# Kernel optimization log

Measured on AMD Instinct MI355X. Metric: run time of the kernel, lower is better.

The kernel has to match this reference:

```python
import jax
import jax.numpy as jnp
import numpy as np
from jax import lax

DIM = 48
HIDDEN = int(DIM * 2.66)  # 127, matches torch int(dim*ffn_expansion_factor)
EPS_LN = 1e-5
EPS_NORM = 1e-12


def conv2d(x, w, groups=1):
    # x: NCHW, w: OIHW, stride 1, SAME padding (all kernels here are 1x1 or 3x3 pad=1)
    return lax.conv_general_dilated(
        x, w, window_strides=(1, 1), padding='SAME',
        feature_group_count=groups,
        dimension_numbers=('NCHW', 'OIHW', 'NCHW'))


def layernorm_cbias(x, w, b):
    # Restormer WithBias_LayerNorm: normalize over channel dim (biased var)
    mu = jnp.mean(x, axis=1, keepdims=True)
    var = jnp.mean(jnp.square(x - mu), axis=1, keepdims=True)
    xn = (x - mu) * lax.rsqrt(var + EPS_LN)
    return xn * w[None, :, None, None] + b[None, :, None, None]


def l2norm_last(x):
    # torch F.normalize(dim=-1, eps=1e-12)
    n = jnp.sqrt(jnp.sum(jnp.square(x), axis=-1, keepdims=True))
    return x / jnp.maximum(n, EPS_NORM)


def setup_inputs() -> dict:
    key = jax.random.key(0)
    ks = jax.random.split(key, 16)
    s = 0.05
    B, H, W = 2, 512, 512
    return {
        'x': jax.random.normal(ks[0], (B, 3, H, W), dtype=jnp.float32),
        # OverlapPatchEmbed: Conv2d(3, 48, 3, pad=1, bias=False)
        'pe_w': jax.random.normal(ks[1], (DIM, 3, 3, 3), dtype=jnp.float32) * s,
        # norm1 (WithBias)
        'n1_w': jnp.ones((DIM,), dtype=jnp.float32),
        'n1_b': jnp.zeros((DIM,), dtype=jnp.float32),
        # MDTA attention, num_heads=1
        'temp': jnp.ones((1, 1, 1), dtype=jnp.float32),
        'qkv_w': jax.random.normal(ks[2], (DIM * 3, DIM, 1, 1), dtype=jnp.float32) * s,
        'qkv_dw_w': jax.random.normal(ks[3], (DIM * 3, 1, 3, 3), dtype=jnp.float32) * s,
        'po_w': jax.random.normal(ks[4], (DIM, DIM, 1, 1), dtype=jnp.float32) * s,
        # norm2
        'n2_w': jnp.ones((DIM,), dtype=jnp.float32),
        'n2_b': jnp.zeros((DIM,), dtype=jnp.float32),
        # GDFN
        'pi_w': jax.random.normal(ks[5], (HIDDEN * 2, DIM, 1, 1), dtype=jnp.float32) * s,
        'ffn_dw_w': jax.random.normal(ks[6], (HIDDEN * 2, 1, 3, 3), dtype=jnp.float32) * s,
        'fo_w': jax.random.normal(ks[7], (DIM, HIDDEN, 1, 1), dtype=jnp.float32) * s,
    }


def reference(x, pe_w, n1_w, n1_b, temp, qkv_w, qkv_dw_w, po_w, n2_w, n2_b, pi_w, ffn_dw_w, fo_w):
    # Patch embed
    patch = conv2d(x, pe_w)  # [B, 48, H, W]
    B, C, H, W = patch.shape

    # ---- MDTA channel attention on norm1(patch) ----
    y = layernorm_cbias(patch, n1_w, n1_b)
    qkv = conv2d(conv2d(y, qkv_w), qkv_dw_w, groups=3 * C)  # [B, 3C, H, W]
    q, k, v = jnp.split(qkv, 3, axis=1)
    # heads=1: rearrange to [B, C, H*W]
    q = l2norm_last(q.reshape(B, C, H * W))
    k = l2norm_last(k.reshape(B, C, H * W))
    v = v.reshape(B, C, H * W)
    attn = jax.nn.softmax(jnp.einsum('bcn,bdn->bcd', q, k) * temp[0, 0, 0], axis=-1)  # [B, C, C]
    out = jnp.einsum('bcd,bdn->bcn', attn, v).reshape(B, C, H, W)
    attn_out = conv2d(out, po_w)
    first = patch + attn_out

    # ---- GDFN on norm2(first) ----
    y2 = layernorm_cbias(first, n2_w, n2_b)
    h = conv2d(conv2d(y2, pi_w), ffn_dw_w, groups=2 * HIDDEN)  # [B, 254, H, W]
    x1, x2 = jnp.split(h, 2, axis=1)
    ffn = conv2d(jax.nn.gelu(x1, approximate=False) * x2, fo_w)
    return first + ffn  # second_residual [B, 48, H, W]
```

## Files before the change

kernel.cpp:

```cpp
#include <hip/hip_runtime.h>
#include <hip/hip_bf16.h>
#include <math.h>

#define HW 512
#define NPIX (HW*HW)

typedef __hip_bfloat16 bf16;
typedef __attribute__((ext_vector_type(8))) unsigned short u16x8;
typedef __attribute__((ext_vector_type(8))) short s16x8;
typedef __attribute__((ext_vector_type(4))) float f32x4;

__device__ __forceinline__ float b2f(bf16 v) { return __bfloat162float(v); }
__device__ __forceinline__ bf16 f2b(float v) { return __float2bfloat16(v); }

union fu { float f; unsigned int u; };
union bu { bf16 b; unsigned short u; };

__device__ __forceinline__ float us2f(unsigned short u) {
    fu c; c.u = ((unsigned int)u) << 16; return c.f;
}

__device__ __forceinline__ void ld_bf8(const bf16* p, float* f) {
    u16x8 u = *(const u16x8*)p;
#pragma unroll
    for (int j = 0; j < 8; j++) { fu c; c.u = ((unsigned int)u[j]) << 16; f[j] = c.f; }
}

__device__ __forceinline__ void st_bf8(bf16* p, const float* f) {
    u16x8 u;
#pragma unroll
    for (int j = 0; j < 8; j++) { bu c; c.b = f2b(f[j]); u[j] = c.u; }
    *(u16x8*)p = u;
}

__global__ __launch_bounds__(256) void k_prep(const float* __restrict__ qkvw,
                                              const float* __restrict__ piw,
                                              const float* __restrict__ fow,
                                              bf16* __restrict__ WQ,
                                              bf16* __restrict__ WP,
                                              bf16* __restrict__ WF,
                                              float* __restrict__ Z0,
                                              float* __restrict__ Z1)
{
    int idx = blockIdx.x*256 + threadIdx.x;
    if (idx < 9216) {
        int oc = idx >> 6, k = idx & 63;
        WQ[idx] = f2b(k < 48 ? qkvw[oc*48 + k] : 0.f);
    } else if (idx < 25600) {
        int j = idx - 9216; int oc = j >> 6, k = j & 63;
        WP[j] = f2b((oc < 254 && k < 48) ? piw[oc*48 + k] : 0.f);
    } else if (idx < 31744) {
        int j = idx - 25600; int oc = j >> 7, k = j & 127;
        WF[j] = f2b(k < 127 ? fow[oc*127 + k] : 0.f);
    } else if (idx < 36544) {
        int j = idx - 31744;
        if (j < 2400) Z0[j] = 0.f; else Z1[j-2400] = 0.f;
    }
}

__global__ __launch_bounds__(256) void k_pe(const float* __restrict__ x,
                                            const float* __restrict__ w,
                                            bf16* __restrict__ out)
{
    __shared__ float ws[48*27];
    for (int i = threadIdx.x; i < 48*27; i += 256) ws[i] = w[i];
    __syncthreads();
    int lane = threadIdx.x & 63, wv = threadIdx.x >> 6;
    int row = blockIdx.x*4 + wv;
    int col = lane*8;
    float a[3][3][8];
    float lf[3][3], rt[3][3];
#pragma unroll
    for (int c = 0; c < 3; c++)
#pragma unroll
        for (int r = 0; r < 3; r++) {
            int rr = row + r - 1;
            if (rr >= 0 && rr < HW) {
                const float* p = x + (size_t)c*NPIX + rr*HW + col;
                float4 u0 = *(const float4*)p, u1 = *(const float4*)(p+4);
                a[c][r][0]=u0.x; a[c][r][1]=u0.y; a[c][r][2]=u0.z; a[c][r][3]=u0.w;
                a[c][r][4]=u1.x; a[c][r][5]=u1.y; a[c][r][6]=u1.z; a[c][r][7]=u1.w;
            } else {
#pragma unroll
                for (int j = 0; j < 8; j++) a[c][r][j] = 0.f;
            }
            float l = __shfl_up(a[c][r][7], 1);  lf[c][r] = (lane==0)  ? 0.f : l;
            float rv= __shfl_down(a[c][r][0],1); rt[c][r] = (lane==63) ? 0.f : rv;
        }
    for (int oc = 0; oc < 48; oc++) {
        float acc[8];
#pragma unroll
        for (int j = 0; j < 8; j++) acc[j] = 0.f;
#pragma unroll
        for (int c = 0; c < 3; c++)
#pragma unroll
            for (int r = 0; r < 3; r++) {
                float w0 = ws[oc*27 + c*9 + r*3 + 0];
                float w1 = ws[oc*27 + c*9 + r*3 + 1];
                float w2 = ws[oc*27 + c*9 + r*3 + 2];
#pragma unroll
                for (int j = 0; j < 8; j++) {
                    float xm = (j==0) ? lf[c][r] : a[c][r][j-1];
                    float x0 = a[c][r][j];
                    float xp = (j==7) ? rt[c][r] : a[c][r][j+1];
                    acc[j] += w0*xm + w1*x0 + w2*xp;
                }
            }
        st_bf8(out + (size_t)oc*NPIX + row*HW + col, acc);
    }
}

#define YPAD 48
#define CHS 408
__global__ __launch_bounds__(256) void k_ln_dw(const bf16* __restrict__ patch,
                                               const float* __restrict__ lnw,
                                               const float* __restrict__ lnb,
                                               const s16x8* __restrict__ wq,
                                               const float* __restrict__ dww,
                                               bf16* __restrict__ outq)
{
    __shared__ unsigned short y_lds[400*YPAD];
    __shared__ unsigned short a_lds[48*CHS];
    int t = threadIdx.x;
    int c0 = blockIdx.x*32, r0 = blockIdx.y*8;

    for (int p = t; p < 400; p += 256) {
        int hr = p/40, hc = p - hr*40;
        int gr = r0 - 1 + hr, gc = c0 - 1 + hc;
        bool ok = (hc < 34) && (gr >= 0) && (gr < HW) && (gc >= 0) && (gc < HW);
        if (ok) {
            int gpx = gr*HW + gc;
            float y[48];
            float mu = 0.f;
#pragma unroll
            for (int i = 0; i < 48; i++) { y[i] = b2f(patch[(size_t)i*NPIX + gpx]); mu += y[i]; }
            mu *= (1.f/48.f);
            float var = 0.f;
#pragma unroll
            for (int i = 0; i < 48; i++) { float d = y[i]-mu; var += d*d; }
            float s = rsqrtf(var*(1.f/48.f) + 1e-5f);
#pragma unroll
            for (int i = 0; i < 48; i++) y[i] = (y[i]-mu)*s*lnw[i] + lnb[i];
#pragma unroll
            for (int kb = 0; kb < 6; kb++) {
                union { u16x8 v; unsigned short us[8]; } pk;
#pragma unroll
                for (int j = 0; j < 8; j++) { bu b; b.b = f2b(y[kb*8+j]); pk.us[j] = b.u; }
                *(u16x8*)&y_lds[p*YPAD + kb*8] = pk.v;
            }
        } else {
            u16x8 z = {0,0,0,0,0,0,0,0};
#pragma unroll
            for (int kb = 0; kb < 6; kb++) *(u16x8*)&y_lds[p*YPAD + kb*8] = z;
        }
    }
    __syncthreads();

    int lane = t & 63, wv = t >> 6;
    int q = lane >> 4, n = lane & 15;
    int ch2 = lane >> 5;
    int idx5 = lane & 31;
    int orow = idx5 >> 2;
    int cg   = idx5 & 3;

#pragma unroll 1
    for (int cc = 0; cc < 3; cc++) {
        s16x8 w0[3], w1[3];
#pragma unroll
        for (int mi = 0; mi < 3; mi++) {
            int oc = (cc*3 + mi)*16 + n;
            w0[mi] = wq[oc*8 + q];
            w1[mi] = wq[oc*8 + 4 + q];
        }
#pragma unroll 1
        for (int nt = wv; nt < 25; nt += 4) {
            int p16 = nt*16;
            s16x8 ya = *(const s16x8*)&y_lds[(p16 + n)*YPAD + q*8];
            s16x8 yb = {0,0,0,0,0,0,0,0};
            if (q < 2) yb = *(const s16x8*)&y_lds[(p16 + n)*YPAD + 32 + q*8];
#pragma unroll
            for (int mi = 0; mi < 3; mi++) {
                f32x4 acc = {0.f, 0.f, 0.f, 0.f};
                acc = __builtin_amdgcn_mfma_f32_16x16x32_bf16(ya, w0[mi], acc, 0, 0, 0);
                acc = __builtin_amdgcn_mfma_f32_16x16x32_bf16(yb, w1[mi], acc, 0, 0, 0);
                union { unsigned short us[4]; ushort4 v; } pk;
#pragma unroll
                for (int r = 0; r < 4; r++) { bu bb; bb.b = f2b(acc[r]); pk.us[r] = bb.u; }
                *(ushort4*)&a_lds[(mi*16 + n)*CHS + p16 + q*4] = pk.v;
            }
        }
        __syncthreads();

#pragma unroll 1
        for (int i = 0; i < 6; i++) {
            int chl = i*8 + wv*2 + ch2;
            int ch  = cc*48 + chl;
            float wk[9];
#pragma unroll
            for (int k = 0; k < 9; k++) wk[k] = dww[ch*9 + k];
            const unsigned short* ap = &a_lds[chl*CHS];
            float win[3][10];
#pragma unroll
            for (int kr = 0; kr < 3; kr++) {
                u16x8 A = *(const u16x8*)&ap[(orow + kr)*40 + cg*8];
                unsigned int B = *(const unsigned int*)&ap[(orow + kr)*40 + cg*8 + 8];
#pragma unroll
                for (int j = 0; j < 8; j++) win[kr][j] = us2f(A[j]);
                win[kr][8] = us2f((unsigned short)(B & 0xffffu));
                win[kr][9] = us2f((unsigned short)(B >> 16));
            }
            u16x8 pk;
#pragma unroll
            for (int j = 0; j < 8; j++) {
                float sm = 0.f;
#pragma unroll
                for (int kr = 0; kr < 3; kr++)
                    sm += wk[kr*3+0]*win[kr][j] + wk[kr*3+1]*win[kr][j+1] + wk[kr*3+2]*win[kr][j+2];
                bu b; b.b = f2b(sm); pk[j] = b.u;
            }
            *(u16x8*)&outq[(size_t)ch*NPIX + (r0 + orow)*HW + c0 + cg*8] = pk;
        }
        __syncthreads();
    }
}

template<int OC_PAD, int OC_REAL, int MT_PER_WAVE>
__global__ __launch_bounds__(256) void k_ln_mm_mfma(const bf16* __restrict__ in,
                                                    const float* __restrict__ lnw,
                                                    const float* __restrict__ lnb,
                                                    const s16x8* __restrict__ wpad,
                                                    bf16* __restrict__ out)
{
    constexpr int NMT = OC_PAD/16;
    __shared__ s16x8 y_lds[256*8];
    __shared__ unsigned short stage[OC_PAD][72];
    int t = threadIdx.x;
    int base = blockIdx.x*256;
    int px = base + t;
    float y[48];
    float mu = 0.f;
#pragma unroll
    for (int i = 0; i < 48; i++) { y[i] = b2f(in[(size_t)i*NPIX + px]); mu += y[i]; }
    mu *= (1.f/48.f);
    float var = 0.f;
#pragma unroll
    for (int i = 0; i < 48; i++) { float d = y[i]-mu; var += d*d; }
    float s = rsqrtf(var*(1.f/48.f) + 1e-5f);
#pragma unroll
    for (int i = 0; i < 48; i++) y[i] = (y[i]-mu)*s*lnw[i] + lnb[i];
#pragma unroll
    for (int kb = 0; kb < 8; kb++) {
        union { s16x8 v; unsigned short us[8]; } pk;
#pragma unroll
        for (int j = 0; j < 8; j++) {
            int c = kb*8 + j;
            bu b; b.b = f2b(c < 48 ? y[c] : 0.f);
            pk.us[j] = (c < 48) ? b.u : (unsigned short)0;
        }
        y_lds[t*8 + (kb ^ (t & 7))] = pk.v;
    }
    __syncthreads();

    int lane = t & 63, wv = t >> 6;
    int q = lane >> 4, n = lane & 15;
    s16x8 a[MT_PER_WAVE][2];
#pragma unroll
    for (int mi = 0; mi < MT_PER_WAVE; mi++) {
        int mt = wv + 4*mi;
        if (mt < NMT) {
            int oc = mt*16 + n;
            a[mi][0] = wpad[oc*8 + q];
            a[mi][1] = wpad[oc*8 + 4 + q];
        }
    }
#pragma unroll 1
    for (int g = 0; g < 4; g++) {
#pragma unroll
        for (int sub = 0; sub < 4; sub++) {
            int nt = g*4 + sub;
            int npx = nt*16 + n;
            s16x8 b0 = y_lds[npx*8 + (q ^ (npx & 7))];
            s16x8 b1 = y_lds[npx*8 + ((4 + q) ^ (npx & 7))];
#pragma unroll
            for (int mi = 0; mi < MT_PER_WAVE; mi++) {
                int mt = wv + 4*mi;
                if (mt >= NMT) continue;
                f32x4 acc = {0.f, 0.f, 0.f, 0.f};
                acc = __builtin_amdgcn_mfma_f32_16x16x32_bf16(b0, a[mi][0], acc, 0, 0, 0);
                acc = __builtin_amdgcn_mfma_f32_16x16x32_bf16(b1, a[mi][1], acc, 0, 0, 0);
                int oc = mt*16 + n;
                union { unsigned short us[4]; ushort4 v; } pk;
#pragma unroll
                for (int r = 0; r < 4; r++) { bu bb; bb.b = f2b(acc[r]); pk.us[r] = bb.u; }
                *(ushort4*)&stage[oc][sub*16 + q*4] = pk.v;
            }
        }
        __syncthreads();
        if (t < OC_REAL) {
            const u16x8* sp = (const u16x8*)stage[t];
            u16x8 c0 = sp[0], c1 = sp[1], c2 = sp[2], c3 = sp[3];
            u16x8 c4 = sp[4], c5 = sp[5], c6 = sp[6], c7 = sp[7];
            u16x8* op = (u16x8*)(out + (size_t)t*NPIX + base + g*64);
            op[0] = c0; op[1] = c1; op[2] = c2; op[3] = c3;
            op[4] = c4; op[5] = c5; op[6] = c6; op[7] = c7;
        }
        __syncthreads();
    }
}

__global__ __launch_bounds__(512) void k_qkt(const bf16* __restrict__ qm,
                                             const bf16* __restrict__ km,
                                             float* __restrict__ S,
                                             float* __restrict__ sumsq)
{
    __shared__ float Sp[8][48][52];
    __shared__ float ssp[8][96];
    int t = threadIdx.x;
    int lane = t & 63, wv = t >> 6;
    int qg = lane >> 4, n = lane & 15;
    size_t px0 = (size_t)(blockIdx.x*8 + wv) * 128 + qg*8;

    f32x4 acc[3][3];
#pragma unroll
    for (int i = 0; i < 3; i++)
#pragma unroll
        for (int j = 0; j < 3; j++) acc[i][j] = (f32x4){0.f, 0.f, 0.f, 0.f};
    float sq[3] = {0.f, 0.f, 0.f}, sk[3] = {0.f, 0.f, 0.f};

#pragma unroll 2
    for (int s = 0; s < 4; s++) {
        size_t p = px0 + s*32;
        s16x8 qa[3], ka[3];
#pragma unroll
        for (int i = 0; i < 3; i++) {
            qa[i] = *(const s16x8*)&qm[(size_t)(16*i + n)*NPIX + p];
            ka[i] = *(const s16x8*)&km[(size_t)(16*i + n)*NPIX + p];
        }
#pragma unroll
        for (int i = 0; i < 3; i++)
#pragma unroll
            for (int j = 0; j < 3; j++)
                acc[i][j] = __builtin_amdgcn_mfma_f32_16x16x32_bf16(qa[i], ka[j], acc[i][j], 0, 0, 0);
#pragma unroll
        for (int i = 0; i < 3; i++) {
            union { s16x8 v; unsigned short us[8]; } uq, uk;
            uq.v = qa[i]; uk.v = ka[i];
#pragma unroll
            for (int j = 0; j < 8; j++) {
                fu cq; cq.u = ((unsigned int)uq.us[j]) << 16; sq[i] += cq.f*cq.f;
                fu ck; ck.u = ((unsigned int)uk.us[j]) << 16; sk[i] += ck.f*ck.f;
            }
        }
    }

#pragma unroll
    for (int i = 0; i < 3; i++)
#pragma unroll
        for (int j = 0; j < 3; j++)
#pragma unroll
            for (int r = 0; r < 4; r++)
                Sp[wv][16*i + qg*4 + r][16*j + n] = acc[i][j][r];
#pragma unroll
    for (int i = 0; i < 3; i++) {
        float a = sq[i], b = sk[i];
        a += __shfl_down(a, 32); a += __shfl_down(a, 16);
        b += __shfl_down(b, 32); b += __shfl_down(b, 16);
        if (lane < 16) { ssp[wv][16*i + lane] = a; ssp[wv][48 + 16*i + lane] = b; }
    }
    __syncthreads();

    for (int idx = t; idx < 2304; idx += 512) {
        int r = idx / 48, c = idx - r*48;
        float v = 0.f;
#pragma unroll
        for (int w = 0; w < 8; w++) v += Sp[w][r][c];
        atomicAdd(&S[idx], v);
    }
    if (t < 96) {
        float v = 0.f;
#pragma unroll
        for (int w = 0; w < 8; w++) v += ssp[w][t];
        atomicAdd(&sumsq[t], v);
    }
}

__global__ __launch_bounds__(256) void k_attn_final(const float* __restrict__ S,
                                                    const float* __restrict__ sumsq,
                                                    const float* __restrict__ po_w,
                                                    const float* __restrict__ temp,
                                                    float* __restrict__ M)
{
    __shared__ float attn[48][48];
    __shared__ float nrm[96];
    int t = threadIdx.x;
    if (t < 96) nrm[t] = fmaxf(sqrtf(sumsq[t]), 1e-12f);
    __syncthreads();
    float tmp = temp[0];
    if (t < 48) {
        float row[48];
        float mx = -1e30f;
#pragma unroll
        for (int d = 0; d < 48; d++) {
            float l = S[t*48+d] / (nrm[t]*nrm[48+d]) * tmp;
            row[d] = l; mx = fmaxf(mx, l);
        }
        float sum = 0.f;
#pragma unroll
        for (int d = 0; d < 48; d++) { float e = expf(row[d]-mx); sum += e; row[d] = e; }
        float inv = 1.f/sum;
#pragma unroll
        for (int d = 0; d < 48; d++) attn[t][d] = row[d]*inv;
    }
    __syncthreads();
    for (int idx = t; idx < 2304; idx += 256) {
        int cp = idx/48, d = idx%48;
        float acc = 0.f;
#pragma unroll
        for (int c = 0; c < 48; c++) acc += po_w[cp*48+c] * attn[c][d];
        M[idx] = acc;
    }
}

__global__ __launch_bounds__(256) void k_attnv(const bf16* __restrict__ v,
                                               const float* __restrict__ M,
                                               bf16* __restrict__ patch)
{
    __shared__ float Ms[48*48];
    for (int i = threadIdx.x; i < 2304; i += 256) Ms[i] = M[i];
    __syncthreads();
    int p = (blockIdx.x*256 + threadIdx.x)*2;
    float v0[48], v1[48];
#pragma unroll
    for (int i = 0; i < 48; i++) {
        unsigned int word = *(const unsigned int*)&v[(size_t)i*NPIX + p];
        fu c0, c1; c0.u = word << 16; c1.u = word & 0xffff0000u;
        v0[i] = c0.f; v1[i] = c1.f;
    }
    for (int oc = 0; oc < 48; oc++) {
        const float4* wr = (const float4*)&Ms[oc*48];
        float a0 = 0.f, a1 = 0.f;
#pragma unroll
        for (int i = 0; i < 12; i++) {
            float4 w4 = wr[i];
            a0 += w4.x*v0[4*i] + w4.y*v0[4*i+1] + w4.z*v0[4*i+2] + w4.w*v0[4*i+3];
            a1 += w4.x*v1[4*i] + w4.y*v1[4*i+1] + w4.z*v1[4*i+2] + w4.w*v1[4*i+3];
        }
        unsigned int* pp = (unsigned int*)&patch[(size_t)oc*NPIX + p];
        unsigned int old = *pp;
        fu f0, f1; f0.u = old << 16; f1.u = old & 0xffff0000u;
        bu b0, b1; b0.b = f2b(f0.f + a0); b1.b = f2b(f1.f + a1);
        *pp = (unsigned int)b0.u | ((unsigned int)b1.u << 16);
    }
}

__global__ __launch_bounds__(256) void k_dw_glu(const bf16* __restrict__ h1,
                                                const float* __restrict__ w,
                                                bf16* __restrict__ g)
{
    int ch = blockIdx.y;
    int lane = threadIdx.x & 63, wv = threadIdx.x >> 6;
    int row0 = blockIdx.x*32 + wv*8;
    int col = lane*8;
    float w1[9], w2[9];
#pragma unroll
    for (int i = 0; i < 9; i++) { w1[i] = w[ch*9+i]; w2[i] = w[(ch+127)*9+i]; }
    const bf16* i1 = h1 + (size_t)ch*NPIX;
    const bf16* i2 = h1 + (size_t)(ch+127)*NPIX;
    bf16* op = g + (size_t)ch*NPIX;
    float aa[3][8], bb[3][8];
    float lfa[3], rta[3], lfb[3], rtb[3];

    auto loadrow = [&](int s, int rr) {
        if (rr >= 0 && rr < HW) {
            ld_bf8(i1 + rr*HW + col, aa[s]);
            ld_bf8(i2 + rr*HW + col, bb[s]);
        } else {
#pragma unroll
            for (int j = 0; j < 8; j++) { aa[s][j] = 0.f; bb[s][j] = 0.f; }
        }
        float l1 = __shfl_up(aa[s][7],1);   lfa[s] = (lane==0)  ? 0.f : l1;
        float r1 = __shfl_down(aa[s][0],1); rta[s] = (lane==63) ? 0.f : r1;
        float l2 = __shfl_up(bb[s][7],1);   lfb[s] = (lane==0)  ? 0.f : l2;
        float r2 = __shfl_down(bb[s][0],1); rtb[s] = (lane==63) ? 0.f : r2;
    };
    loadrow(0, row0-1);
    loadrow(1, row0);
#pragma unroll
    for (int r = 0; r < 8; r++) {
        loadrow((r+2)%3, row0 + r + 1);
        const int s0 = r%3, s1 = (r+1)%3, s2 = (r+2)%3;
        float o[8];
#pragma unroll
        for (int j = 0; j < 8; j++) {
            float sum1 = 0.f, sum2 = 0.f;
#pragma unroll
            for (int kr = 0; kr < 3; kr++) {
                const int ss = (kr==0) ? s0 : (kr==1) ? s1 : s2;
                float xm = (j==0) ? lfa[ss] : aa[ss][j-1];
                float x0 = aa[ss][j];
                float xp = (j==7) ? rta[ss] : aa[ss][j+1];
                sum1 += w1[kr*3+0]*xm + w1[kr*3+1]*x0 + w1[kr*3+2]*xp;
                float ym = (j==0) ? lfb[ss] : bb[ss][j-1];
                float y0 = bb[ss][j];
                float yp = (j==7) ? rtb[ss] : bb[ss][j+1];
                sum2 += w2[kr*3+0]*ym + w2[kr*3+1]*y0 + w2[kr*3+2]*yp;
            }
            float ge = 0.5f*sum1*(1.f + erff(sum1*0.70710678118654752f));
            o[j] = ge*sum2;
        }
        st_bf8(op + (row0 + r)*HW + col, o);
    }
}

__global__ __launch_bounds__(256) void k_fo_mfma(const bf16* __restrict__ g,
                                                 const s16x8* __restrict__ wfo,
                                                 const bf16* __restrict__ first,
                                                 float* __restrict__ out)
{
    __shared__ s16x8 glds[256*16];
    int t = threadIdx.x;
    int base = blockIdx.x*256;
    int px = base + t;
#pragma unroll
    for (int kb = 0; kb < 16; kb++) {
        union { s16x8 v; unsigned short us[8]; } pk;
#pragma unroll
        for (int j = 0; j < 8; j++) {
            int c = kb*8 + j;
            if (c < 127) { bu b; b.b = g[(size_t)c*NPIX + px]; pk.us[j] = b.u; }
            else pk.us[j] = 0;
        }
        glds[t*16 + (kb ^ (t & 15))] = pk.v;
    }
    __syncthreads();
    int lane = t & 63, wv = t >> 6;
    int q = lane >> 4, n = lane & 15;
    s16x8 a[3][4];
#pragma unroll
    for (int mt = 0; mt < 3; mt++) {
        int oc = mt*16 + n;
#pragma unroll
        for (int kc = 0; kc < 4; kc++)
            a[mt][kc] = wfo[oc*16 + kc*4 + q];
    }
#pragma unroll 1
    for (int ni = 0; ni < 4; ni++) {
        int nt = wv*4 + ni;
        int npx = nt*16 + n;
        s16x8 b[4];
#pragma unroll
        for (int kc = 0; kc < 4; kc++)
            b[kc] = glds[npx*16 + ((kc*4 + q) ^ (npx & 15))];
        size_t px4 = (size_t)base + nt*16 + q*4;
#pragma unroll
        for (int mt = 0; mt < 3; mt++) {
            f32x4 acc = {0.f, 0.f, 0.f, 0.f};
#pragma unroll
            for (int kc = 0; kc < 4; kc++)
                acc = __builtin_amdgcn_mfma_f32_16x16x32_bf16(b[kc], a[mt][kc], acc, 0, 0, 0);
            int oc = mt*16 + n;
            ushort4 fr = *(const ushort4*)&first[(size_t)oc*NPIX + px4];
            float4 o;
            o.x = us2f(fr.x) + acc[0];
            o.y = us2f(fr.y) + acc[1];
            o.z = us2f(fr.z) + acc[2];
            o.w = us2f(fr.w) + acc[3];
            *(float4*)&out[(size_t)oc*NPIX + px4] = o;
        }
    }
}

extern "C" void kernel_launch(void* const* d_in, const int* in_sizes, int n_in,
                              void* d_out, int out_size, void* d_ws, size_t ws_size,
                              hipStream_t stream)
{
    const float* x     = (const float*)d_in[0];
    const float* pe_w  = (const float*)d_in[1];
    const float* n1w   = (const float*)d_in[2];
    const float* n1b   = (const float*)d_in[3];
    const float* temp  = (const float*)d_in[4];
    const float* qkvw  = (const float*)d_in[5];
    const float* qkvdw = (const float*)d_in[6];
    const float* pow_  = (const float*)d_in[7];
    const float* n2w   = (const float*)d_in[8];
    const float* n2b   = (const float*)d_in[9];
    const float* piw   = (const float*)d_in[10];
    const float* ffndw = (const float*)d_in[11];
    const float* fow   = (const float*)d_in[12];
    float* out = (float*)d_out;

    bf16*  Pb = (bf16*)d_ws;
    bf16*  A  = Pb + (size_t)48*NPIX;
    bf16*  Bq = A + (size_t)144*NPIX;
    bf16*  H1 = A;
    bf16*  G  = A + (size_t)254*NPIX;
    bf16*  WQ = A + (size_t)381*NPIX;
    bf16*  WP = WQ + 144*64;
    bf16*  WF = WP + 256*64;
    float* SM0 = (float*)(A + (size_t)384*NPIX);
    float* SM1 = SM0 + 4704;

    dim3 blk(256);
    int nb1 = NPIX/256;
    int nb2 = NPIX/512;
    int nr  = HW/4;
    int nrw = HW/32;

    k_prep<<<dim3(143), blk, 0, stream>>>(qkvw, piw, fow, WQ, WP, WF, SM0, SM1);

    for (int b = 0; b < 2; b++) {
        const float* xb   = x   + (size_t)b*3*NPIX;
        float*       outb = out + (size_t)b*48*NPIX;
        float* SMb   = b ? SM1 : SM0;
        float* sumsq = SMb;
        float* S     = SMb + 96;
        float* M     = SMb + 2400;

        k_pe<<<dim3(nr), blk, 0, stream>>>(xb, pe_w, Pb);
        k_ln_dw<<<dim3(HW/32, HW/8), blk, 0, stream>>>(Pb, n1w, n1b, (const s16x8*)WQ, qkvdw, Bq);
        k_qkt<<<dim3(NPIX/1024), dim3(512), 0, stream>>>(Bq, Bq + (size_t)48*NPIX, S, sumsq);
        k_attn_final<<<dim3(1), blk, 0, stream>>>(S, sumsq, pow_, temp, M);
        k_attnv<<<dim3(nb2), blk, 0, stream>>>(Bq + (size_t)96*NPIX, M, Pb);
        k_ln_mm_mfma<256,254,4><<<dim3(nb1), blk, 0, stream>>>(Pb, n2w, n2b, (const s16x8*)WP, H1);
        k_dw_glu<<<dim3(nrw, 127), blk, 0, stream>>>(H1, ffndw, G);
        k_fo_mfma<<<dim3(nb1), blk, 0, stream>>>(G, (const s16x8*)WF, Pb, outb);
    }
}
```

Measured before the change: 749.3 us.

## Fuse depthwise GLU conv with output projection MFMA via LDS tile

Merges the depthwise 3x3 conv + GELU gating kernel with the fo 1x1 MFMA projection. Each block computes the gated hidden values for a 32x8 pixel tile across all 127 channels into shared memory, then runs the MFMA projection and residual add directly. This removes the round trip of the 127-channel intermediate G through global memory and one launch. In exchange it adds halo loads at tile edges, a large LDS footprint (~67KB) that limits occupancy, and strided LDS gathers for the B operand that may cause bank conflicts.

```diff
diff --git a/kernel.cpp b/kernel.cpp
--- a/kernel.cpp
+++ b/kernel.cpp
@@ -453,87 +453,90 @@
     }
 }
 
-__global__ __launch_bounds__(256) void k_dw_glu(const bf16* __restrict__ h1,
+#define GCHS 264
+__global__ __launch_bounds__(256) void k_glu_fo(const bf16* __restrict__ h1,
                                                 const float* __restrict__ w,
-                                                bf16* __restrict__ g)
-{
-    int ch = blockIdx.y;
-    int lane = threadIdx.x & 63, wv = threadIdx.x >> 6;
-    int row0 = blockIdx.x*32 + wv*8;
-    int col = lane*8;
-    float w1[9], w2[9];
-#pragma unroll
-    for (int i = 0; i < 9; i++) { w1[i] = w[ch*9+i]; w2[i] = w[(ch+127)*9+i]; }
-    const bf16* i1 = h1 + (size_t)ch*NPIX;
-    const bf16* i2 = h1 + (size_t)(ch+127)*NPIX;
-    bf16* op = g + (size_t)ch*NPIX;
-    float aa[3][8], bb[3][8];
-    float lfa[3], rta[3], lfb[3], rtb[3];
-
-    auto loadrow = [&](int s, int rr) {
-        if (rr >= 0 && rr < HW) {
-            ld_bf8(i1 + rr*HW + col, aa[s]);
-            ld_bf8(i2 + rr*HW + col, bb[s]);
-        } else {
-#pragma unroll
-            for (int j = 0; j < 8; j++) { aa[s][j] = 0.f; bb[s][j] = 0.f; }
-        }
-        float l1 = __shfl_up(aa[s][7],1);   lfa[s] = (lane==0)  ? 0.f : l1;
-        float r1 = __shfl_down(aa[s][0],1); rta[s] = (lane==63) ? 0.f : r1;
-        float l2 = __shfl_up(bb[s][7],1);   lfb[s] = (lane==0)  ? 0.f : l2;
-        float r2 = __shfl_down(bb[s][0],1); rtb[s] = (lane==63) ? 0.f : r2;
-    };
-    loadrow(0, row0-1);
-    loadrow(1, row0);
-#pragma unroll
-    for (int r = 0; r < 8; r++) {
-        loadrow((r+2)%3, row0 + r + 1);
-        const int s0 = r%3, s1 = (r+1)%3, s2 = (r+2)%3;
-        float o[8];
+                                                const s16x8* __restrict__ wfo,
+                                                const bf16* __restrict__ first,
+                                                float* __restrict__ out)
+{
+    __shared__ unsigned short g_lds[128*GCHS];
+    int t = threadIdx.x;
+    int lane = t & 63, wv = t >> 6;
+    int c0 = blockIdx.x*32, r0 = blockIdx.y*8;
+
+    int ch2 = lane >> 5;
+    int idx5 = lane & 31;
+    int orow = idx5 >> 2;
+    int cg   = idx5 & 3;
+    int col  = c0 + cg*8;
+
+#pragma unroll 1
+    for (int i = 0; i < 16; i++) {
+        int ch = i*8 + wv*2 + ch2;
+        bool valid = (ch < 127);
+        float w1[9], w2[9];
+#pragma unroll
+        for (int k = 0; k < 9; k++) {
+            w1[k] = valid ? w[ch*9+k] : 0.f;
+            w2[k] = valid ? w[(ch+127)*9+k] : 0.f;
+        }
+        const bf16* i1 = h1 + (size_t)(valid ? ch : 0)*NPIX;
+        const bf16* i2 = h1 + (size_t)(valid ? (ch+127) : 0)*NPIX;
+        float aa[3][8], bb[3][8];
+        float lfa[3], rta[3], lfb[3], rtb[3];
+#pragma unroll
+        for (int kr = 0; kr < 3; kr++) {
+            int rr = r0 + orow + kr - 1;
+            bool rok = (rr >= 0 && rr < HW);
+            if (rok) {
+                ld_bf8(i1 + rr*HW + col, aa[kr]);
+                ld_bf8(i2 + rr*HW + col, bb[kr]);
+            } else {
+#pragma unroll
+                for (int j = 0; j < 8; j++) { aa[kr][j] = 0.f; bb[kr][j] = 0.f; }
+            }
+            float l1 = __shfl_up(aa[kr][7], 1), l2 = __shfl_up(bb[kr][7], 1);
+            if (cg == 0) {
+                l1 = 0.f; l2 = 0.f;
+                if (col > 0 && rok) {
+                    l1 = b2f(i1[rr*HW + col - 1]);
+                    l2 = b2f(i2[rr*HW + col - 1]);
+                }
+            }
+            lfa[kr] = l1; lfb[kr] = l2;
+            float r1 = __shfl_down(aa[kr][0], 1), r2 = __shfl_down(bb[kr][0], 1);
+            if (cg == 3) {
+                r1 = 0.f; r2 = 0.f;
+                if (col + 8 < HW && rok) {
+                    r1 = b2f(i1[rr*HW + col + 8]);
+                    r2 = b2f(i2[rr*HW + col + 8]);
+                }
+            }
+            rta[kr] = r1; rtb[kr] = r2;
+        }
+        u16x8 pk;
 #pragma unroll
         for (int j = 0; j < 8; j++) {
-            float sum1 = 0.f, sum2 = 0.f;
+            float s1 = 0.f, s2 = 0.f;
 #pragma unroll
             for (int kr = 0; kr < 3; kr++) {
-                const int ss = (kr==0) ? s0 : (kr==1) ? s1 : s2;
-                float xm = (j==0) ? lfa[ss] : aa[ss][j-1];
-                float x0 = aa[ss][j];
-                float xp = (j==7) ? rta[ss] : aa[ss][j+1];
-                sum1 += w1[kr*3+0]*xm + w1[kr*3+1]*x0 + w1[kr*3+2]*xp;
-                float ym = (j==0) ? lfb[ss] : bb[ss][j-1];
-                float y0 = bb[ss][j];
-                float yp = (j==7) ? rtb[ss] : bb[ss][j+1];
-                sum2 += w2[kr*3+0]*ym + w2[kr*3+1]*y0 + w2[kr*3+2]*yp;
-            }
-            float ge = 0.5f*sum1*(1.f + erff(sum1*0.70710678118654752f));
-            o[j] = ge*sum2;
-        }
-        st_bf8(op + (row0 + r)*HW + col, o);
-    }
-}
-
-__global__ __launch_bounds__(256) void k_fo_mfma(const bf16* __restrict__ g,
-                                                 const s16x8* __restrict__ wfo,
-                                                 const bf16* __restrict__ first,
-                                                 float* __restrict__ out)
-{
-    __shared__ s16x8 glds[256*16];
-    int t = threadIdx.x;
-    int base = blockIdx.x*256;
-    int px = base + t;
-#pragma unroll
-    for (int kb = 0; kb < 16; kb++) {
-        union { s16x8 v; unsigned short us[8]; } pk;
-#pragma unroll
-        for (int j = 0; j < 8; j++) {
-            int c = kb*8 + j;
-            if (c < 127) { bu b; b.b = g[(size_t)c*NPIX + px]; pk.us[j] = b.u; }
-            else pk.us[j] = 0;
-        }
-        glds[t*16 + (kb ^ (t & 15))] = pk.v;
-    }
-    __syncthreads();
-    int lane = t & 63, wv = t >> 6;
+                float xm = (j==0) ? lfa[kr] : aa[kr][j-1];
+                float x0 = aa[kr][j];
+                float xp = (j==7) ? rta[kr] : aa[kr][j+1];
+                s1 += w1[kr*3+0]*xm + w1[kr*3+1]*x0 + w1[kr*3+2]*xp;
+                float ym = (j==0) ? lfb[kr] : bb[kr][j-1];
+                float y0 = bb[kr][j];
+                float yp = (j==7) ? rtb[kr] : bb[kr][j+1];
+                s2 += w2[kr*3+0]*ym + w2[kr*3+1]*y0 + w2[kr*3+2]*yp;
+            }
+            float ge = 0.5f*s1*(1.f + erff(s1*0.70710678118654752f));
+            bu b; b.b = f2b(ge*s2); pk[j] = b.u;
+        }
+        *(u16x8*)&g_lds[ch*GCHS + orow*32 + cg*8] = pk;
+    }
+    __syncthreads();
+
     int q = lane >> 4, n = lane & 15;
     s16x8 a[3][4];
 #pragma unroll
@@ -546,12 +549,17 @@
 #pragma unroll 1
     for (int ni = 0; ni < 4; ni++) {
         int nt = wv*4 + ni;
-        int npx = nt*16 + n;
         s16x8 b[4];
 #pragma unroll
-        for (int kc = 0; kc < 4; kc++)
-            b[kc] = glds[npx*16 + ((kc*4 + q) ^ (npx & 15))];
-        size_t px4 = (size_t)base + nt*16 + q*4;
+        for (int kc = 0; kc < 4; kc++) {
+            union { s16x8 v; unsigned short us[8]; } f;
+#pragma unroll
+            for (int j = 0; j < 8; j++)
+                f.us[j] = g_lds[(kc*32 + q*8 + j)*GCHS + nt*16 + n];
+            b[kc] = f.v;
+        }
+        int px4 = nt*16 + q*4;
+        size_t gbase = (size_t)(r0 + (px4 >> 5))*HW + c0 + (px4 & 31);
 #pragma unroll
         for (int mt = 0; mt < 3; mt++) {
             f32x4 acc = {0.f, 0.f, 0.f, 0.f};
@@ -559,13 +567,13 @@
             for (int kc = 0; kc < 4; kc++)
                 acc = __builtin_amdgcn_mfma_f32_16x16x32_bf16(b[kc], a[mt][kc], acc, 0, 0, 0);
             int oc = mt*16 + n;
-            ushort4 fr = *(const ushort4*)&first[(size_t)oc*NPIX + px4];
+            ushort4 fr = *(const ushort4*)&first[(size_t)oc*NPIX + gbase];
             float4 o;
             o.x = us2f(fr.x) + acc[0];
             o.y = us2f(fr.y) + acc[1];
             o.z = us2f(fr.z) + acc[2];
             o.w = us2f(fr.w) + acc[3];
-            *(float4*)&out[(size_t)oc*NPIX + px4] = o;
+            *(float4*)&out[(size_t)oc*NPIX + gbase] = o;
         }
     }
 }
@@ -593,7 +601,6 @@
     bf16*  A  = Pb + (size_t)48*NPIX;
     bf16*  Bq = A + (size_t)144*NPIX;
     bf16*  H1 = A;
-    bf16*  G  = A + (size_t)254*NPIX;
     bf16*  WQ = A + (size_t)381*NPIX;
     bf16*  WP = WQ + 144*64;
     bf16*  WF = WP + 256*64;
@@ -604,7 +611,6 @@
     int nb1 = NPIX/256;
     int nb2 = NPIX/512;
     int nr  = HW/4;
-    int nrw = HW/32;
 
     k_prep<<<dim3(143), blk, 0, stream>>>(qkvw, piw, fow, WQ, WP, WF, SM0, SM1);
 
@@ -622,7 +628,6 @@
         k_attn_final<<<dim3(1), blk, 0, stream>>>(S, sumsq, pow_, temp, M);
         k_attnv<<<dim3(nb2), blk, 0, stream>>>(Bq + (size_t)96*NPIX, M, Pb);
         k_ln_mm_mfma<256,254,4><<<dim3(nb1), blk, 0, stream>>>(Pb, n2w, n2b, (const s16x8*)WP, H1);
-        k_dw_glu<<<dim3(nrw, 127), blk, 0, stream>>>(H1, ffndw, G);
-        k_fo_mfma<<<dim3(nb1), blk, 0, stream>>>(G, (const s16x8*)WF, Pb, outb);
-    }
-}
+        k_glu_fo<<<dim3(HW/32, HW/8), blk, 0, stream>>>(H1, ffndw, (const s16x8*)WF, Pb, outb);
+    }
+}
```

Result: slower. 863.1 us (+15.2%).
